# Performance work log

Hardware: AMD Instinct MI355X
Metric: run time of the kernel (lower is better)

## Reference

```python
import jax, jax.numpy as jnp
import numpy as np
import math

B, S, H, N = 1, 4096, 1024, 16
HN = H // N  # 64

def setup_inputs() -> dict:
    key = jax.random.key(0)
    k1, k2, k3 = jax.random.split(key, 3)
    hidden_states = jax.random.normal(k1, (B, S, H), dtype=jnp.float32)
    # lower-triangular causal mask, float {0,1}, broadcastable to [b,np,s,s]
    ltor_mask = jnp.tril(jnp.ones((1, 1, S, S), dtype=jnp.float32))
    w_qkv = jax.random.normal(k2, (3 * H, H), dtype=jnp.float32) * 0.02
    b_qkv = jnp.zeros((3 * H,), dtype=jnp.float32)
    w_dense = jax.random.normal(k3, (H, H), dtype=jnp.float32) * 0.02
    b_dense = jnp.zeros((H,), dtype=jnp.float32)
    return {"hidden_states": hidden_states, "ltor_mask": ltor_mask,
            "w_qkv": w_qkv, "b_qkv": b_qkv,
            "w_dense": w_dense, "b_dense": b_dense}

def reference(hidden_states, ltor_mask, w_qkv, b_qkv, w_dense, b_dense):
    b, s, h = hidden_states.shape
    # fused QKV projection: [b,s,3h]
    mixed = jnp.einsum('bsh,oh->bso', hidden_states, w_qkv) + b_qkv
    q, k, v = jnp.split(mixed, 3, axis=-1)
    # [b,s,h] -> [b,n,s,hn]
    def heads(t):
        return t.reshape(b, s, N, HN).transpose(0, 2, 1, 3)
    q, k, v = heads(q), heads(k), heads(v)
    # raw scores [b,n,s,s]
    scores = jnp.einsum('bnqd,bnkd->bnqk', q, k) / math.sqrt(HN)
    # multiplicative mask plus -10000 additive for masked positions
    scores = scores * ltor_mask - 10000.0 * (1.0 - ltor_mask)
    probs = jax.nn.softmax(scores, axis=-1)
    # attention dropout prob = 0.0 -> identity
    ctx = jnp.einsum('bnqk,bnkd->bnqd', probs, v)
    ctx = ctx.transpose(0, 2, 1, 3).reshape(b, s, h)
    out = jnp.einsum('bsh,oh->bso', ctx, w_dense) + b_dense
    # output dropout prob = 0.0 -> identity
    return out
```

## Files before the change

### kernel.cpp

```cpp
#include <hip/hip_runtime.h>
#include <hip/hip_bf16.h>

static constexpr int SEQ  = 4096;
static constexpr int HID  = 1024;
static constexpr int NHEAD = 16;
static constexpr int HDIM  = 64;
static constexpr int H3   = 3072;

typedef __attribute__((ext_vector_type(8))) __bf16 bf16x8;
typedef __attribute__((ext_vector_type(4))) float  f32x4;

__device__ __forceinline__ float bf2f(unsigned short u) {
    union { unsigned int u; float f; } v; v.u = ((unsigned int)u) << 16; return v.f;
}
__device__ __forceinline__ unsigned short f2bf(float f) {
    union { float f; unsigned int u; } v; v.f = f;
    unsigned int r = v.u + 0x7fffu + ((v.u >> 16) & 1u);
    return (unsigned short)(r >> 16);
}
__device__ __forceinline__ void gl_lds16(const unsigned short* g, unsigned short* l) {
    __builtin_amdgcn_global_load_lds(
        (const __attribute__((address_space(1))) void*)g,
        (__attribute__((address_space(3))) void*)l, 16, 0, 0);
}

struct Conv5 { const float* src[5]; unsigned short* dst[5]; };

__global__ __launch_bounds__(256) void convert5(Conv5 c) {
    constexpr int cnt[5]  = {4194304, 3145728, 3072, 1048576, 1024};
    constexpr int boff[5] = {0, 2048, 3584, 3586, 4098};
    const int b = blockIdx.x;
    int t = 0, rel = b;
#pragma unroll
    for (int k = 1; k < 5; ++k) if (b >= boff[k]) { t = k; rel = b - boff[k]; }
    const int base = rel * 2048 + threadIdx.x * 8;
    if (base >= cnt[t]) return;
    const float* s = c.src[t] + base;
    const float4 a = ((const float4*)s)[0];
    const float4 b2 = ((const float4*)s)[1];
    union { unsigned short v[8]; uint4 q; } u;
    u.v[0] = f2bf(a.x); u.v[1] = f2bf(a.y); u.v[2] = f2bf(a.z); u.v[3] = f2bf(a.w);
    u.v[4] = f2bf(b2.x); u.v[5] = f2bf(b2.y); u.v[6] = f2bf(b2.z); u.v[7] = f2bf(b2.w);
    *(uint4*)(c.dst[t] + base) = u.q;
}

template <int BM, int BN, int BK, typename OutT, bool VFUSE>
__global__ __launch_bounds__(256) void gemm_bt(
    const unsigned short* __restrict__ A, const unsigned short* __restrict__ B,
    const unsigned short* __restrict__ bias, OutT* __restrict__ C,
    unsigned short* __restrict__ vt,
    int M, int N, int K)
{
    constexpr int MI  = BM / 32;
    constexpr int NI  = BN / 32;
    constexpr int KC  = BK / 32;
    constexpr int CB  = BK / 8;
    constexpr int LSH = (BK == 32) ? 2 : 3;
    constexpr int RPC = 64 >> LSH;

    const int tid  = threadIdx.x;
    const int wave = tid >> 6, lane = tid & 63;
    const int quad = lane >> 4, c16 = lane & 15;
    const int m0 = blockIdx.y * BM, n0 = blockIdx.x * BN;
    const int wr = wave >> 1, wc = wave & 1;

    __shared__ __align__(16) unsigned short sA[BM * BK];
    __shared__ __align__(16) unsigned short sB[BN * BK];

    f32x4 acc[MI][NI];
#pragma unroll
    for (int i = 0; i < MI; ++i)
#pragma unroll
        for (int j = 0; j < NI; ++j) acc[i][j] = {0.f, 0.f, 0.f, 0.f};

    const int sr = lane >> LSH;
    const int sc = ((lane & (CB - 1)) ^ (sr & (CB - 1))) * 8;

    for (int k0 = 0; k0 < K; k0 += BK) {
#pragma unroll
        for (int cc = 0; cc < BM / RPC / 4; ++cc) {
            const int rbase = cc * (4 * RPC) + wave * RPC;
            gl_lds16(A + (size_t)(m0 + rbase + sr) * K + k0 + sc, &sA[rbase * BK]);
        }
#pragma unroll
        for (int cc = 0; cc < BN / RPC / 4; ++cc) {
            const int rbase = cc * (4 * RPC) + wave * RPC;
            gl_lds16(B + (size_t)(n0 + rbase + sr) * K + k0 + sc, &sB[rbase * BK]);
        }
        __syncthreads();

#pragma unroll
        for (int kc = 0; kc < KC; ++kc) {
            bf16x8 af[MI], bfr[NI];
#pragma unroll
            for (int i = 0; i < MI; ++i) {
                const int ra = wr * (BM / 2) + i * 16 + c16;
                af[i] = *(const bf16x8*)&sA[ra * BK + (((kc * 4 + quad) ^ ra) & (CB - 1)) * 8];
            }
#pragma unroll
            for (int j = 0; j < NI; ++j) {
                const int rb = wc * (BN / 2) + j * 16 + c16;
                bfr[j] = *(const bf16x8*)&sB[rb * BK + (((kc * 4 + quad) ^ rb) & (CB - 1)) * 8];
            }
#pragma unroll
            for (int i = 0; i < MI; ++i)
#pragma unroll
                for (int j = 0; j < NI; ++j)
                    acc[i][j] = __builtin_amdgcn_mfma_f32_16x16x32_bf16(af[i], bfr[j], acc[i][j], 0, 0, 0);
        }
        __syncthreads();
    }

    if constexpr (VFUSE) {
        if (n0 >= 2048) {
#pragma unroll
            for (int j = 0; j < NI; ++j) {
                const int col = n0 + wc * (BN / 2) + j * 16 + c16;
                const float bv = bf2f(bias[col]);
                const int d  = col - 2048;
                unsigned short* vrow = vt + (size_t)d * SEQ;
#pragma unroll
                for (int i = 0; i < MI; ++i) {
                    const int base32 = m0 + wr * (BM / 2) + (i >> 1) * 32;
                    const int phys = base32 + 8 * quad + 4 * (i & 1);
                    union { unsigned short u[4]; uint2 q2; } w;
#pragma unroll
                    for (int r = 0; r < 4; ++r) w.u[r] = f2bf(acc[i][j][r] + bv);
                    *(uint2*)&vrow[phys] = w.q2;
                }
            }
            return;
        }
    }

#pragma unroll
    for (int j = 0; j < NI; ++j) {
        const int col = n0 + wc * (BN / 2) + j * 16 + c16;
        const float bv = bf2f(bias[col]);
#pragma unroll
        for (int i = 0; i < MI; ++i) {
#pragma unroll
            for (int r = 0; r < 4; ++r) {
                const int row = m0 + wr * (BM / 2) + i * 16 + quad * 4 + r;
                const float v = acc[i][j][r] + bv;
                if constexpr (sizeof(OutT) == 2) C[(size_t)row * N + col] = (OutT)f2bf(v);
                else                             C[(size_t)row * N + col] = (OutT)v;
            }
        }
    }
}

__global__ __launch_bounds__(256) void attn_causal(
    const unsigned short* __restrict__ qkv, const unsigned short* __restrict__ vt,
    unsigned short* __restrict__ ctx)
{
    const int bx = blockIdx.x;
    const int n  = bx & 15;
    const int p  = bx >> 4;
    const int tid  = threadIdx.x;
    const int wave = tid >> 6, lane = tid & 63;
    const int quad = lane >> 4, c16 = lane & 15;
    const int qg  = wave & 1;
    const int kvh = wave >> 1;

    __shared__ __align__(16) unsigned short smem[16384];
    unsigned short* smem_k = smem;
    unsigned short* smem_v = smem + 8192;

    const float QS = 0.125f * 1.44269504f;
    const int srow8 = lane >> 3;
    const int scol8 = ((lane & 7) ^ (lane >> 3)) * 8;
    const int srow4 = lane >> 4;

#pragma unroll 1
    for (int t = 0; t < 2; ++t) {
        const int z = t ? p : 63 - p;
        const int qrow0 = z * 64 + qg * 32;

        bf16x8 qf[2][2];
#pragma unroll
        for (int wq = 0; wq < 2; ++wq)
#pragma unroll
            for (int kc = 0; kc < 2; ++kc) {
                bf16x8 q = *(const bf16x8*)(qkv + (size_t)(qrow0 + wq * 16 + c16) * H3 + n * HDIM + kc * 32 + quad * 8);
#pragma unroll
                for (int j = 0; j < 8; ++j) q[j] = (__bf16)((float)q[j] * QS);
                qf[wq][kc] = q;
            }

        f32x4 o[2][4];
#pragma unroll
        for (int wq = 0; wq < 2; ++wq)
#pragma unroll
            for (int dt = 0; dt < 4; ++dt) o[wq][dt] = {0.f, 0.f, 0.f, 0.f};
        float l_i[2] = {0.f, 0.f};

        const int nkb = (z + 2) >> 1;
        for (int kb = 0; kb < nkb; ++kb) {
            const int kv0 = kb * 128;
#pragma unroll
            for (int cc = 0; cc < 4; ++cc) {
                const int rb = wave * 32 + cc * 8;
                gl_lds16(qkv + (size_t)(kv0 + rb + srow8) * H3 + HID + n * HDIM + scol8,
                         &smem_k[rb * 64]);
            }
#pragma unroll
            for (int cc = 0; cc < 4; ++cc) {
                const int rb = wave * 16 + cc * 4;
                const int sv = (((lane & 15) ^ ((cc * 4 + srow4) & 15))) * 8;
                gl_lds16(vt + (size_t)(n * HDIM + rb + srow4) * SEQ + kv0 + sv,
                         &smem_v[rb * 128]);
            }
            __syncthreads();

            const int kv0w = kv0 + kvh * 64;
            if (kv0w <= qrow0 + 31) {
                f32x4 s[2][4];
#pragma unroll
                for (int wq = 0; wq < 2; ++wq)
#pragma unroll
                    for (int mt = 0; mt < 4; ++mt) s[wq][mt] = {0.f, 0.f, 0.f, 0.f};
#pragma unroll
                for (int mt = 0; mt < 4; ++mt) {
                    const int krow = kvh * 64 + mt * 16 + c16;
                    const bf16x8 kf0 = *(const bf16x8*)&smem_k[krow * 64 + ((quad)     ^ (krow & 7)) * 8];
                    const bf16x8 kf1 = *(const bf16x8*)&smem_k[krow * 64 + ((4 + quad) ^ (krow & 7)) * 8];
#pragma unroll
                    for (int wq = 0; wq < 2; ++wq) {
                        s[wq][mt] = __builtin_amdgcn_mfma_f32_16x16x32_bf16(kf0, qf[wq][0], s[wq][mt], 0, 0, 0);
                        s[wq][mt] = __builtin_amdgcn_mfma_f32_16x16x32_bf16(kf1, qf[wq][1], s[wq][mt], 0, 0, 0);
                    }
                }

#pragma unroll
                for (int wq = 0; wq < 2; ++wq) {
                    if (kv0w + 63 > qrow0 + wq * 16) {
                        const int q_g = qrow0 + wq * 16 + c16;
#pragma unroll
                        for (int mt = 0; mt < 4; ++mt)
#pragma unroll
                            for (int r = 0; r < 4; ++r) {
                                const int kv = kv0w + mt * 16 + quad * 4 + r;
                                if (kv > q_g) s[wq][mt][r] = -30000.0f;
                            }
                    }
                    float rs = 0.f;
#pragma unroll
                    for (int mt = 0; mt < 4; ++mt)
#pragma unroll
                        for (int r = 0; r < 4; ++r) {
                            const float pp = __builtin_amdgcn_exp2f(s[wq][mt][r]);
                            s[wq][mt][r] = pp;
                            rs += pp;
                        }
                    l_i[wq] += rs;
                }

                bf16x8 pf[2][2];
#pragma unroll
                for (int wq = 0; wq < 2; ++wq)
#pragma unroll
                    for (int kc = 0; kc < 2; ++kc) {
                        union { __bf16 b[8]; bf16x8 v; } pp;
#pragma unroll
                        for (int r = 0; r < 4; ++r) {
                            pp.b[r]     = (__bf16)s[wq][2 * kc][r];
                            pp.b[4 + r] = (__bf16)s[wq][2 * kc + 1][r];
                        }
                        pf[wq][kc] = pp.v;
                    }

#pragma unroll
                for (int kc = 0; kc < 2; ++kc) {
#pragma unroll
                    for (int dt = 0; dt < 4; ++dt) {
                        const int vrow = dt * 16 + c16;
                        const int pc8 = (kvh * 8 + kc * 4 + quad) ^ (vrow & 15);
                        const bf16x8 vf = *(const bf16x8*)&smem_v[vrow * 128 + pc8 * 8];
#pragma unroll
                        for (int wq = 0; wq < 2; ++wq)
                            o[wq][dt] = __builtin_amdgcn_mfma_f32_16x16x32_bf16(vf, pf[wq][kc], o[wq][dt], 0, 0, 0);
                    }
                }
            }
            __syncthreads();
        }

#pragma unroll
        for (int wq = 0; wq < 2; ++wq) {
            l_i[wq] += __shfl_xor(l_i[wq], 16);
            l_i[wq] += __shfl_xor(l_i[wq], 32);
        }

        float* cb = (float*)smem;
        float* lb = (float*)(smem + 8704);
        unsigned short* fb = smem + 8832;

        if (kvh == 0) {
#pragma unroll
            for (int wq = 0; wq < 2; ++wq) {
#pragma unroll
                for (int dt = 0; dt < 4; ++dt)
                    *(f32x4*)&cb[(qg * 32 + wq * 16 + c16) * 68 + dt * 16 + quad * 4] = o[wq][dt];
                if (quad == 0) lb[qg * 32 + wq * 16 + c16] = l_i[wq];
            }
        }
        __syncthreads();
        if (kvh == 1) {
#pragma unroll
            for (int wq = 0; wq < 2; ++wq) {
                const float inv = 1.0f / (l_i[wq] + lb[qg * 32 + wq * 16 + c16]);
#pragma unroll
                for (int dt = 0; dt < 4; ++dt) {
                    const f32x4 pv = *(const f32x4*)&cb[(qg * 32 + wq * 16 + c16) * 68 + dt * 16 + quad * 4];
                    union { unsigned short u[4]; uint2 q2; } w;
#pragma unroll
                    for (int r = 0; r < 4; ++r) w.u[r] = f2bf((o[wq][dt][r] + pv[r]) * inv);
                    *(uint2*)&fb[(qg * 32 + wq * 16 + c16) * 72 + dt * 16 + quad * 4] = w.q2;
                }
            }
        }
        __syncthreads();

        const int qr = tid >> 2;
        const int xc = (tid & 3) * 16;
        unsigned short* dst = ctx + (size_t)(z * 64 + qr) * HID + n * HDIM + xc;
        *(uint4*)dst       = *(const uint4*)&fb[qr * 72 + xc];
        *(uint4*)(dst + 8) = *(const uint4*)&fb[qr * 72 + xc + 8];

        __syncthreads();
    }
}

extern "C" void kernel_launch(void* const* d_in, const int* in_sizes, int n_in,
                              void* d_out, int out_size, void* d_ws, size_t ws_size,
                              hipStream_t stream)
{
    unsigned short* base = (unsigned short*)d_ws;

    unsigned short* hs_c = base;
    unsigned short* wq_c = hs_c + 4194304;
    unsigned short* bq_c = wq_c + 3145728;
    unsigned short* wd_c = bq_c + 3072;
    unsigned short* bd_c = wd_c + 1048576;
    unsigned short* qkv  = bd_c + 1024;
    unsigned short* vt   = qkv + (size_t)SEQ * H3;
    unsigned short* ctx  = hs_c;

    Conv5 c;
    c.src[0] = (const float*)d_in[0]; c.src[1] = (const float*)d_in[2];
    c.src[2] = (const float*)d_in[3]; c.src[3] = (const float*)d_in[4];
    c.src[4] = (const float*)d_in[5];
    c.dst[0] = hs_c; c.dst[1] = wq_c; c.dst[2] = bq_c; c.dst[3] = wd_c; c.dst[4] = bd_c;
    hipLaunchKernelGGL(convert5, dim3(4099), dim3(256), 0, stream, c);

    hipLaunchKernelGGL((gemm_bt<128, 128, 32, unsigned short, true>),
                       dim3(H3 / 128, SEQ / 128), dim3(256), 0, stream,
                       hs_c, wq_c, bq_c, qkv, vt, SEQ, H3, HID);
    hipLaunchKernelGGL(attn_causal, dim3(NHEAD * (SEQ / 128)), dim3(256), 0, stream,
                       qkv, vt, ctx);
    hipLaunchKernelGGL((gemm_bt<64, 128, 64, float, false>),
                       dim3(HID / 128, SEQ / 64), dim3(256), 0, stream,
                       ctx, wd_c, bd_c, (float*)d_out, (unsigned short*)nullptr, SEQ, HID, HID);
}
```

Before: 248.0 us.

## Drop LDS staging in attention, one query tile per block, deeper QKV GEMM K-tile

The attention kernel stops staging K and V tiles in shared memory behind block-wide barriers. Each wave now reads its K and V fragments straight from global memory, and each wave loops only over the key blocks its causal range needs, so waves no longer synchronise per key block. Each block now handles a single 64-row query tile instead of a balanced pair, which doubles the grid, and the tile order is remapped so heavy and light tiles interleave. The QKV GEMM K-tile is raised from 32 to 64. The risk is lower reuse of K and V, more global and L2 traffic, and uncoalesced strided loads.

```diff
diff --git a/kernel.cpp b/kernel.cpp
--- a/kernel.cpp
+++ b/kernel.cpp
@@ -156,180 +156,156 @@
 {
     const int bx = blockIdx.x;
     const int n  = bx & 15;
-    const int p  = bx >> 4;
+    const int z0 = bx >> 4;
+    const int z  = (z0 < 32) ? z0 : 95 - z0;
     const int tid  = threadIdx.x;
     const int wave = tid >> 6, lane = tid & 63;
     const int quad = lane >> 4, c16 = lane & 15;
     const int qg  = wave & 1;
     const int kvh = wave >> 1;
 
-    __shared__ __align__(16) unsigned short smem[16384];
-    unsigned short* smem_k = smem;
-    unsigned short* smem_v = smem + 8192;
+    __shared__ __align__(16) unsigned short smem[13440];
+
+    const int qrow0 = z * 64 + qg * 32;
 
     const float QS = 0.125f * 1.44269504f;
-    const int srow8 = lane >> 3;
-    const int scol8 = ((lane & 7) ^ (lane >> 3)) * 8;
-    const int srow4 = lane >> 4;
-
-#pragma unroll 1
-    for (int t = 0; t < 2; ++t) {
-        const int z = t ? p : 63 - p;
-        const int qrow0 = z * 64 + qg * 32;
-
-        bf16x8 qf[2][2];
+    bf16x8 qf[2][2];
+#pragma unroll
+    for (int wq = 0; wq < 2; ++wq)
+#pragma unroll
+        for (int kc = 0; kc < 2; ++kc) {
+            bf16x8 q = *(const bf16x8*)(qkv + (size_t)(qrow0 + wq * 16 + c16) * H3 + n * HDIM + kc * 32 + quad * 8);
+#pragma unroll
+            for (int j = 0; j < 8; ++j) q[j] = (__bf16)((float)q[j] * QS);
+            qf[wq][kc] = q;
+        }
+
+    f32x4 o[2][4];
+#pragma unroll
+    for (int wq = 0; wq < 2; ++wq)
+#pragma unroll
+        for (int dt = 0; dt < 4; ++dt) o[wq][dt] = {0.f, 0.f, 0.f, 0.f};
+    float l_i[2] = {0.f, 0.f};
+
+    const int Lq  = qrow0 + 31;
+    const int rel = Lq - kvh * 64;
+    const int nkb = (rel >= 0) ? (rel >> 7) + 1 : 0;
+
+    const unsigned short* kbase = qkv + HID + n * HDIM;
+    const unsigned short* vbase = vt + (size_t)(n * HDIM) * SEQ;
+
+    for (int kb = 0; kb < nkb; ++kb) {
+        const int kv0w = kb * 128 + kvh * 64;
+
+        f32x4 s[2][4];
 #pragma unroll
         for (int wq = 0; wq < 2; ++wq)
 #pragma unroll
+            for (int mt = 0; mt < 4; ++mt) s[wq][mt] = {0.f, 0.f, 0.f, 0.f};
+#pragma unroll
+        for (int mt = 0; mt < 4; ++mt) {
+            const unsigned short* kp = kbase + (size_t)(kv0w + mt * 16 + c16) * H3 + quad * 8;
+            const bf16x8 kf0 = *(const bf16x8*)kp;
+            const bf16x8 kf1 = *(const bf16x8*)(kp + 32);
+#pragma unroll
+            for (int wq = 0; wq < 2; ++wq) {
+                s[wq][mt] = __builtin_amdgcn_mfma_f32_16x16x32_bf16(kf0, qf[wq][0], s[wq][mt], 0, 0, 0);
+                s[wq][mt] = __builtin_amdgcn_mfma_f32_16x16x32_bf16(kf1, qf[wq][1], s[wq][mt], 0, 0, 0);
+            }
+        }
+
+#pragma unroll
+        for (int wq = 0; wq < 2; ++wq) {
+            if (kv0w + 63 > qrow0 + wq * 16) {
+                const int q_g = qrow0 + wq * 16 + c16;
+#pragma unroll
+                for (int mt = 0; mt < 4; ++mt)
+#pragma unroll
+                    for (int r = 0; r < 4; ++r) {
+                        const int kv = kv0w + mt * 16 + quad * 4 + r;
+                        if (kv > q_g) s[wq][mt][r] = -30000.0f;
+                    }
+            }
+            float rs = 0.f;
+#pragma unroll
+            for (int mt = 0; mt < 4; ++mt)
+#pragma unroll
+                for (int r = 0; r < 4; ++r) {
+                    const float pp = __builtin_amdgcn_exp2f(s[wq][mt][r]);
+                    s[wq][mt][r] = pp;
+                    rs += pp;
+                }
+            l_i[wq] += rs;
+        }
+
+        bf16x8 pf[2][2];
+#pragma unroll
+        for (int wq = 0; wq < 2; ++wq)
+#pragma unroll
             for (int kc = 0; kc < 2; ++kc) {
-                bf16x8 q = *(const bf16x8*)(qkv + (size_t)(qrow0 + wq * 16 + c16) * H3 + n * HDIM + kc * 32 + quad * 8);
-#pragma unroll
-                for (int j = 0; j < 8; ++j) q[j] = (__bf16)((float)q[j] * QS);
-                qf[wq][kc] = q;
-            }
-
-        f32x4 o[2][4];
-#pragma unroll
-        for (int wq = 0; wq < 2; ++wq)
-#pragma unroll
-            for (int dt = 0; dt < 4; ++dt) o[wq][dt] = {0.f, 0.f, 0.f, 0.f};
-        float l_i[2] = {0.f, 0.f};
-
-        const int nkb = (z + 2) >> 1;
-        for (int kb = 0; kb < nkb; ++kb) {
-            const int kv0 = kb * 128;
-#pragma unroll
-            for (int cc = 0; cc < 4; ++cc) {
-                const int rb = wave * 32 + cc * 8;
-                gl_lds16(qkv + (size_t)(kv0 + rb + srow8) * H3 + HID + n * HDIM + scol8,
-                         &smem_k[rb * 64]);
-            }
-#pragma unroll
-            for (int cc = 0; cc < 4; ++cc) {
-                const int rb = wave * 16 + cc * 4;
-                const int sv = (((lane & 15) ^ ((cc * 4 + srow4) & 15))) * 8;
-                gl_lds16(vt + (size_t)(n * HDIM + rb + srow4) * SEQ + kv0 + sv,
-                         &smem_v[rb * 128]);
-            }
-            __syncthreads();
-
-            const int kv0w = kv0 + kvh * 64;
-            if (kv0w <= qrow0 + 31) {
-                f32x4 s[2][4];
+                union { __bf16 b[8]; bf16x8 v; } pp;
+#pragma unroll
+                for (int r = 0; r < 4; ++r) {
+                    pp.b[r]     = (__bf16)s[wq][2 * kc][r];
+                    pp.b[4 + r] = (__bf16)s[wq][2 * kc + 1][r];
+                }
+                pf[wq][kc] = pp.v;
+            }
+
+#pragma unroll
+        for (int kc = 0; kc < 2; ++kc) {
+#pragma unroll
+            for (int dt = 0; dt < 4; ++dt) {
+                const int vrow = dt * 16 + c16;
+                const bf16x8 vf = *(const bf16x8*)(vbase + (size_t)vrow * SEQ + kv0w + kc * 32 + quad * 8);
 #pragma unroll
                 for (int wq = 0; wq < 2; ++wq)
-#pragma unroll
-                    for (int mt = 0; mt < 4; ++mt) s[wq][mt] = {0.f, 0.f, 0.f, 0.f};
-#pragma unroll
-                for (int mt = 0; mt < 4; ++mt) {
-                    const int krow = kvh * 64 + mt * 16 + c16;
-                    const bf16x8 kf0 = *(const bf16x8*)&smem_k[krow * 64 + ((quad)     ^ (krow & 7)) * 8];
-                    const bf16x8 kf1 = *(const bf16x8*)&smem_k[krow * 64 + ((4 + quad) ^ (krow & 7)) * 8];
-#pragma unroll
-                    for (int wq = 0; wq < 2; ++wq) {
-                        s[wq][mt] = __builtin_amdgcn_mfma_f32_16x16x32_bf16(kf0, qf[wq][0], s[wq][mt], 0, 0, 0);
-                        s[wq][mt] = __builtin_amdgcn_mfma_f32_16x16x32_bf16(kf1, qf[wq][1], s[wq][mt], 0, 0, 0);
-                    }
-                }
-
-#pragma unroll
-                for (int wq = 0; wq < 2; ++wq) {
-                    if (kv0w + 63 > qrow0 + wq * 16) {
-                        const int q_g = qrow0 + wq * 16 + c16;
-#pragma unroll
-                        for (int mt = 0; mt < 4; ++mt)
-#pragma unroll
-                            for (int r = 0; r < 4; ++r) {
-                                const int kv = kv0w + mt * 16 + quad * 4 + r;
-                                if (kv > q_g) s[wq][mt][r] = -30000.0f;
-                            }
-                    }
-                    float rs = 0.f;
-#pragma unroll
-                    for (int mt = 0; mt < 4; ++mt)
-#pragma unroll
-                        for (int r = 0; r < 4; ++r) {
-                            const float pp = __builtin_amdgcn_exp2f(s[wq][mt][r]);
-                            s[wq][mt][r] = pp;
-                            rs += pp;
-                        }
-                    l_i[wq] += rs;
-                }
-
-                bf16x8 pf[2][2];
-#pragma unroll
-                for (int wq = 0; wq < 2; ++wq)
-#pragma unroll
-                    for (int kc = 0; kc < 2; ++kc) {
-                        union { __bf16 b[8]; bf16x8 v; } pp;
-#pragma unroll
-                        for (int r = 0; r < 4; ++r) {
-                            pp.b[r]     = (__bf16)s[wq][2 * kc][r];
-                            pp.b[4 + r] = (__bf16)s[wq][2 * kc + 1][r];
-                        }
-                        pf[wq][kc] = pp.v;
-                    }
-
-#pragma unroll
-                for (int kc = 0; kc < 2; ++kc) {
-#pragma unroll
-                    for (int dt = 0; dt < 4; ++dt) {
-                        const int vrow = dt * 16 + c16;
-                        const int pc8 = (kvh * 8 + kc * 4 + quad) ^ (vrow & 15);
-                        const bf16x8 vf = *(const bf16x8*)&smem_v[vrow * 128 + pc8 * 8];
-#pragma unroll
-                        for (int wq = 0; wq < 2; ++wq)
-                            o[wq][dt] = __builtin_amdgcn_mfma_f32_16x16x32_bf16(vf, pf[wq][kc], o[wq][dt], 0, 0, 0);
-                    }
-                }
-            }
-            __syncthreads();
-        }
-
+                    o[wq][dt] = __builtin_amdgcn_mfma_f32_16x16x32_bf16(vf, pf[wq][kc], o[wq][dt], 0, 0, 0);
+            }
+        }
+    }
+
+#pragma unroll
+    for (int wq = 0; wq < 2; ++wq) {
+        l_i[wq] += __shfl_xor(l_i[wq], 16);
+        l_i[wq] += __shfl_xor(l_i[wq], 32);
+    }
+
+    float* cb = (float*)smem;
+    float* lb = (float*)(smem + 8704);
+    unsigned short* fb = smem + 8832;
+
+    if (kvh == 0) {
 #pragma unroll
         for (int wq = 0; wq < 2; ++wq) {
-            l_i[wq] += __shfl_xor(l_i[wq], 16);
-            l_i[wq] += __shfl_xor(l_i[wq], 32);
-        }
-
-        float* cb = (float*)smem;
-        float* lb = (float*)(smem + 8704);
-        unsigned short* fb = smem + 8832;
-
-        if (kvh == 0) {
-#pragma unroll
-            for (int wq = 0; wq < 2; ++wq) {
-#pragma unroll
-                for (int dt = 0; dt < 4; ++dt)
-                    *(f32x4*)&cb[(qg * 32 + wq * 16 + c16) * 68 + dt * 16 + quad * 4] = o[wq][dt];
-                if (quad == 0) lb[qg * 32 + wq * 16 + c16] = l_i[wq];
-            }
-        }
-        __syncthreads();
-        if (kvh == 1) {
-#pragma unroll
-            for (int wq = 0; wq < 2; ++wq) {
-                const float inv = 1.0f / (l_i[wq] + lb[qg * 32 + wq * 16 + c16]);
-#pragma unroll
-                for (int dt = 0; dt < 4; ++dt) {
-                    const f32x4 pv = *(const f32x4*)&cb[(qg * 32 + wq * 16 + c16) * 68 + dt * 16 + quad * 4];
-                    union { unsigned short u[4]; uint2 q2; } w;
-#pragma unroll
-                    for (int r = 0; r < 4; ++r) w.u[r] = f2bf((o[wq][dt][r] + pv[r]) * inv);
-                    *(uint2*)&fb[(qg * 32 + wq * 16 + c16) * 72 + dt * 16 + quad * 4] = w.q2;
-                }
-            }
-        }
-        __syncthreads();
-
-        const int qr = tid >> 2;
-        const int xc = (tid & 3) * 16;
-        unsigned short* dst = ctx + (size_t)(z * 64 + qr) * HID + n * HDIM + xc;
-        *(uint4*)dst       = *(const uint4*)&fb[qr * 72 + xc];
-        *(uint4*)(dst + 8) = *(const uint4*)&fb[qr * 72 + xc + 8];
-
-        __syncthreads();
-    }
+#pragma unroll
+            for (int dt = 0; dt < 4; ++dt)
+                *(f32x4*)&cb[(qg * 32 + wq * 16 + c16) * 68 + dt * 16 + quad * 4] = o[wq][dt];
+            if (quad == 0) lb[qg * 32 + wq * 16 + c16] = l_i[wq];
+        }
+    }
+    __syncthreads();
+    if (kvh == 1) {
+#pragma unroll
+        for (int wq = 0; wq < 2; ++wq) {
+            const float inv = 1.0f / (l_i[wq] + lb[qg * 32 + wq * 16 + c16]);
+#pragma unroll
+            for (int dt = 0; dt < 4; ++dt) {
+                const f32x4 pv = *(const f32x4*)&cb[(qg * 32 + wq * 16 + c16) * 68 + dt * 16 + quad * 4];
+                union { unsigned short u[4]; uint2 q2; } w;
+#pragma unroll
+                for (int r = 0; r < 4; ++r) w.u[r] = f2bf((o[wq][dt][r] + pv[r]) * inv);
+                *(uint2*)&fb[(qg * 32 + wq * 16 + c16) * 72 + dt * 16 + quad * 4] = w.q2;
+            }
+        }
+    }
+    __syncthreads();
+
+    const int qr = tid >> 2;
+    const int xc = (tid & 3) * 16;
+    unsigned short* dst = ctx + (size_t)(z * 64 + qr) * HID + n * HDIM + xc;
+    *(uint4*)dst       = *(const uint4*)&fb[qr * 72 + xc];
+    *(uint4*)(dst + 8) = *(const uint4*)&fb[qr * 72 + xc + 8];
 }
 
 extern "C" void kernel_launch(void* const* d_in, const int* in_sizes, int n_in,
@@ -354,10 +330,10 @@
     c.dst[0] = hs_c; c.dst[1] = wq_c; c.dst[2] = bq_c; c.dst[3] = wd_c; c.dst[4] = bd_c;
     hipLaunchKernelGGL(convert5, dim3(4099), dim3(256), 0, stream, c);
 
-    hipLaunchKernelGGL((gemm_bt<128, 128, 32, unsigned short, true>),
+    hipLaunchKernelGGL((gemm_bt<128, 128, 64, unsigned short, true>),
                        dim3(H3 / 128, SEQ / 128), dim3(256), 0, stream,
                        hs_c, wq_c, bq_c, qkv, vt, SEQ, H3, HID);
-    hipLaunchKernelGGL(attn_causal, dim3(NHEAD * (SEQ / 128)), dim3(256), 0, stream,
+    hipLaunchKernelGGL(attn_causal, dim3(NHEAD * (SEQ / 64)), dim3(256), 0, stream,
                        qkv, vt, ctx);
     hipLaunchKernelGGL((gemm_bt<64, 128, 64, float, false>),
                        dim3(HID / 128, SEQ / 64), dim3(256), 0, stream,
```

Measured after the change: 307.5 us. 1.24x slower.

## Double-buffer K/V tiles in attention, one query tile per block, raise QKV GEMM BK

Applied to the files above, without the earlier changes.

The attention kernel now launches one block per 64-row query tile, where each block previously handled a paired long and short tile. Blocks are ordered heaviest-first. K/V tiles are double-buffered in LDS so the next tile's global-to-LDS load is issued before computing on the current one, which removes one barrier per iteration. The MFMA sections get raised wave priority with s_setprio. The QKV GEMM K-tile grows from 32 to 64. The changes aim to overlap load latency with compute and improve load balance, at the cost of doubled LDS use (64KB per block), which may lower occupancy.

```diff
diff --git a/kernel.cpp b/kernel.cpp
--- a/kernel.cpp
+++ b/kernel.cpp
@@ -156,180 +156,188 @@
 {
     const int bx = blockIdx.x;
     const int n  = bx & 15;
-    const int p  = bx >> 4;
+    const int z  = 63 - (bx >> 4);
     const int tid  = threadIdx.x;
     const int wave = tid >> 6, lane = tid & 63;
     const int quad = lane >> 4, c16 = lane & 15;
     const int qg  = wave & 1;
     const int kvh = wave >> 1;
 
-    __shared__ __align__(16) unsigned short smem[16384];
-    unsigned short* smem_k = smem;
-    unsigned short* smem_v = smem + 8192;
+    __shared__ __align__(16) unsigned short smem[32768];
+
+    const int qrow0 = z * 64 + qg * 32;
 
     const float QS = 0.125f * 1.44269504f;
+    bf16x8 qf[2][2];
+#pragma unroll
+    for (int wq = 0; wq < 2; ++wq)
+#pragma unroll
+        for (int kc = 0; kc < 2; ++kc) {
+            bf16x8 q = *(const bf16x8*)(qkv + (size_t)(qrow0 + wq * 16 + c16) * H3 + n * HDIM + kc * 32 + quad * 8);
+#pragma unroll
+            for (int j = 0; j < 8; ++j) q[j] = (__bf16)((float)q[j] * QS);
+            qf[wq][kc] = q;
+        }
+
+    f32x4 o[2][4];
+#pragma unroll
+    for (int wq = 0; wq < 2; ++wq)
+#pragma unroll
+        for (int dt = 0; dt < 4; ++dt) o[wq][dt] = {0.f, 0.f, 0.f, 0.f};
+    float l_i[2] = {0.f, 0.f};
+
     const int srow8 = lane >> 3;
     const int scol8 = ((lane & 7) ^ (lane >> 3)) * 8;
     const int srow4 = lane >> 4;
 
-#pragma unroll 1
-    for (int t = 0; t < 2; ++t) {
-        const int z = t ? p : 63 - p;
-        const int qrow0 = z * 64 + qg * 32;
-
-        bf16x8 qf[2][2];
-#pragma unroll
-        for (int wq = 0; wq < 2; ++wq)
+    const int NK = (z + 2) >> 1;
+
+    auto stage = [&](int t, int kb) {
+        unsigned short* sk = smem + t * 16384;
+        unsigned short* sv = sk + 8192;
+        const int kv0 = kb * 128;
+#pragma unroll
+        for (int cc = 0; cc < 4; ++cc) {
+            const int rb = wave * 32 + cc * 8;
+            gl_lds16(qkv + (size_t)(kv0 + rb + srow8) * H3 + HID + n * HDIM + scol8,
+                     &sk[rb * 64]);
+        }
+#pragma unroll
+        for (int cc = 0; cc < 4; ++cc) {
+            const int rb = wave * 16 + cc * 4;
+            const int sv8 = (((lane & 15) ^ ((cc * 4 + srow4) & 15))) * 8;
+            gl_lds16(vt + (size_t)(n * HDIM + rb + srow4) * SEQ + kv0 + sv8,
+                     &sv[rb * 128]);
+        }
+    };
+
+    stage(0, 0);
+    __syncthreads();
+
+    for (int kb = 0; kb < NK; ++kb) {
+        if (kb + 1 < NK) stage((kb + 1) & 1, kb + 1);
+
+        unsigned short* smem_k = smem + (kb & 1) * 16384;
+        unsigned short* smem_v = smem_k + 8192;
+
+        const int kv0w = kb * 128 + kvh * 64;
+        if (kv0w <= qrow0 + 31) {
+            f32x4 s[2][4];
+#pragma unroll
+            for (int wq = 0; wq < 2; ++wq)
+#pragma unroll
+                for (int mt = 0; mt < 4; ++mt) s[wq][mt] = {0.f, 0.f, 0.f, 0.f};
+            __builtin_amdgcn_s_setprio(1);
+#pragma unroll
+            for (int mt = 0; mt < 4; ++mt) {
+                const int krow = kvh * 64 + mt * 16 + c16;
+                const bf16x8 kf0 = *(const bf16x8*)&smem_k[krow * 64 + ((quad)     ^ (krow & 7)) * 8];
+                const bf16x8 kf1 = *(const bf16x8*)&smem_k[krow * 64 + ((4 + quad) ^ (krow & 7)) * 8];
+#pragma unroll
+                for (int wq = 0; wq < 2; ++wq) {
+                    s[wq][mt] = __builtin_amdgcn_mfma_f32_16x16x32_bf16(kf0, qf[wq][0], s[wq][mt], 0, 0, 0);
+                    s[wq][mt] = __builtin_amdgcn_mfma_f32_16x16x32_bf16(kf1, qf[wq][1], s[wq][mt], 0, 0, 0);
+                }
+            }
+            __builtin_amdgcn_s_setprio(0);
+
+#pragma unroll
+            for (int wq = 0; wq < 2; ++wq) {
+                if (kv0w + 63 > qrow0 + wq * 16) {
+                    const int q_g = qrow0 + wq * 16 + c16;
+#pragma unroll
+                    for (int mt = 0; mt < 4; ++mt)
+#pragma unroll
+                        for (int r = 0; r < 4; ++r) {
+                            const int kv = kv0w + mt * 16 + quad * 4 + r;
+                            if (kv > q_g) s[wq][mt][r] = -30000.0f;
+                        }
+                }
+                float rs = 0.f;
+#pragma unroll
+                for (int mt = 0; mt < 4; ++mt)
+#pragma unroll
+                    for (int r = 0; r < 4; ++r) {
+                        const float pp = __builtin_amdgcn_exp2f(s[wq][mt][r]);
+                        s[wq][mt][r] = pp;
+                        rs += pp;
+                    }
+                l_i[wq] += rs;
+            }
+
+            bf16x8 pf[2][2];
+#pragma unroll
+            for (int wq = 0; wq < 2; ++wq)
+#pragma unroll
+                for (int kc = 0; kc < 2; ++kc) {
+                    union { __bf16 b[8]; bf16x8 v; } pp;
+#pragma unroll
+                    for (int r = 0; r < 4; ++r) {
+                        pp.b[r]     = (__bf16)s[wq][2 * kc][r];
+                        pp.b[4 + r] = (__bf16)s[wq][2 * kc + 1][r];
+                    }
+                    pf[wq][kc] = pp.v;
+                }
+
+            __builtin_amdgcn_s_setprio(1);
 #pragma unroll
             for (int kc = 0; kc < 2; ++kc) {
-                bf16x8 q = *(const bf16x8*)(qkv + (size_t)(qrow0 + wq * 16 + c16) * H3 + n * HDIM + kc * 32 + quad * 8);
-#pragma unroll
-                for (int j = 0; j < 8; ++j) q[j] = (__bf16)((float)q[j] * QS);
-                qf[wq][kc] = q;
-            }
-
-        f32x4 o[2][4];
-#pragma unroll
-        for (int wq = 0; wq < 2; ++wq)
-#pragma unroll
-            for (int dt = 0; dt < 4; ++dt) o[wq][dt] = {0.f, 0.f, 0.f, 0.f};
-        float l_i[2] = {0.f, 0.f};
-
-        const int nkb = (z + 2) >> 1;
-        for (int kb = 0; kb < nkb; ++kb) {
-            const int kv0 = kb * 128;
-#pragma unroll
-            for (int cc = 0; cc < 4; ++cc) {
-                const int rb = wave * 32 + cc * 8;
-                gl_lds16(qkv + (size_t)(kv0 + rb + srow8) * H3 + HID + n * HDIM + scol8,
-                         &smem_k[rb * 64]);
-            }
-#pragma unroll
-            for (int cc = 0; cc < 4; ++cc) {
-                const int rb = wave * 16 + cc * 4;
-                const int sv = (((lane & 15) ^ ((cc * 4 + srow4) & 15))) * 8;
-                gl_lds16(vt + (size_t)(n * HDIM + rb + srow4) * SEQ + kv0 + sv,
-                         &smem_v[rb * 128]);
-            }
-            __syncthreads();
-
-            const int kv0w = kv0 + kvh * 64;
-            if (kv0w <= qrow0 + 31) {
-                f32x4 s[2][4];
-#pragma unroll
-                for (int wq = 0; wq < 2; ++wq)
-#pragma unroll
-                    for (int mt = 0; mt < 4; ++mt) s[wq][mt] = {0.f, 0.f, 0.f, 0.f};
-#pragma unroll
-                for (int mt = 0; mt < 4; ++mt) {
-                    const int krow = kvh * 64 + mt * 16 + c16;
-                    const bf16x8 kf0 = *(const bf16x8*)&smem_k[krow * 64 + ((quad)     ^ (krow & 7)) * 8];
-                    const bf16x8 kf1 = *(const bf16x8*)&smem_k[krow * 64 + ((4 + quad) ^ (krow & 7)) * 8];
-#pragma unroll
-                    for (int wq = 0; wq < 2; ++wq) {
-                        s[wq][mt] = __builtin_amdgcn_mfma_f32_16x16x32_bf16(kf0, qf[wq][0], s[wq][mt], 0, 0, 0);
-                        s[wq][mt] = __builtin_amdgcn_mfma_f32_16x16x32_bf16(kf1, qf[wq][1], s[wq][mt], 0, 0, 0);
-                    }
-                }
-
-#pragma unroll
-                for (int wq = 0; wq < 2; ++wq) {
-                    if (kv0w + 63 > qrow0 + wq * 16) {
-                        const int q_g = qrow0 + wq * 16 + c16;
-#pragma unroll
-                        for (int mt = 0; mt < 4; ++mt)
-#pragma unroll
-                            for (int r = 0; r < 4; ++r) {
-                                const int kv = kv0w + mt * 16 + quad * 4 + r;
-                                if (kv > q_g) s[wq][mt][r] = -30000.0f;
-                            }
-                    }
-                    float rs = 0.f;
-#pragma unroll
-                    for (int mt = 0; mt < 4; ++mt)
-#pragma unroll
-                        for (int r = 0; r < 4; ++r) {
-                            const float pp = __builtin_amdgcn_exp2f(s[wq][mt][r]);
-                            s[wq][mt][r] = pp;
-                            rs += pp;
-                        }
-                    l_i[wq] += rs;
-                }
-
-                bf16x8 pf[2][2];
-#pragma unroll
-                for (int wq = 0; wq < 2; ++wq)
-#pragma unroll
-                    for (int kc = 0; kc < 2; ++kc) {
-                        union { __bf16 b[8]; bf16x8 v; } pp;
-#pragma unroll
-                        for (int r = 0; r < 4; ++r) {
-                            pp.b[r]     = (__bf16)s[wq][2 * kc][r];
-                            pp.b[4 + r] = (__bf16)s[wq][2 * kc + 1][r];
-                        }
-                        pf[wq][kc] = pp.v;
-                    }
-
-#pragma unroll
-                for (int kc = 0; kc < 2; ++kc) {
-#pragma unroll
-                    for (int dt = 0; dt < 4; ++dt) {
-                        const int vrow = dt * 16 + c16;
-                        const int pc8 = (kvh * 8 + kc * 4 + quad) ^ (vrow & 15);
-                        const bf16x8 vf = *(const bf16x8*)&smem_v[vrow * 128 + pc8 * 8];
-#pragma unroll
-                        for (int wq = 0; wq < 2; ++wq)
-                            o[wq][dt] = __builtin_amdgcn_mfma_f32_16x16x32_bf16(vf, pf[wq][kc], o[wq][dt], 0, 0, 0);
-                    }
-                }
-            }
-            __syncthreads();
-        }
-
+#pragma unroll
+                for (int dt = 0; dt < 4; ++dt) {
+                    const int vrow = dt * 16 + c16;
+                    const int pc8 = (kvh * 8 + kc * 4 + quad) ^ (vrow & 15);
+                    const bf16x8 vf = *(const bf16x8*)&smem_v[vrow * 128 + pc8 * 8];
+#pragma unroll
+                    for (int wq = 0; wq < 2; ++wq)
+                        o[wq][dt] = __builtin_amdgcn_mfma_f32_16x16x32_bf16(vf, pf[wq][kc], o[wq][dt], 0, 0, 0);
+                }
+            }
+            __builtin_amdgcn_s_setprio(0);
+        }
+        __syncthreads();
+    }
+
+#pragma unroll
+    for (int wq = 0; wq < 2; ++wq) {
+        l_i[wq] += __shfl_xor(l_i[wq], 16);
+        l_i[wq] += __shfl_xor(l_i[wq], 32);
+    }
+
+    float* cb = (float*)smem;
+    float* lb = (float*)(smem + 8704);
+    unsigned short* fb = smem + 8832;
+
+    if (kvh == 0) {
 #pragma unroll
         for (int wq = 0; wq < 2; ++wq) {
-            l_i[wq] += __shfl_xor(l_i[wq], 16);
-            l_i[wq] += __shfl_xor(l_i[wq], 32);
-        }
-
-        float* cb = (float*)smem;
-        float* lb = (float*)(smem + 8704);
-        unsigned short* fb = smem + 8832;
-
-        if (kvh == 0) {
-#pragma unroll
-            for (int wq = 0; wq < 2; ++wq) {
-#pragma unroll
-                for (int dt = 0; dt < 4; ++dt)
-                    *(f32x4*)&cb[(qg * 32 + wq * 16 + c16) * 68 + dt * 16 + quad * 4] = o[wq][dt];
-                if (quad == 0) lb[qg * 32 + wq * 16 + c16] = l_i[wq];
-            }
-        }
-        __syncthreads();
-        if (kvh == 1) {
-#pragma unroll
-            for (int wq = 0; wq < 2; ++wq) {
-                const float inv = 1.0f / (l_i[wq] + lb[qg * 32 + wq * 16 + c16]);
-#pragma unroll
-                for (int dt = 0; dt < 4; ++dt) {
-                    const f32x4 pv = *(const f32x4*)&cb[(qg * 32 + wq * 16 + c16) * 68 + dt * 16 + quad * 4];
-                    union { unsigned short u[4]; uint2 q2; } w;
-#pragma unroll
-                    for (int r = 0; r < 4; ++r) w.u[r] = f2bf((o[wq][dt][r] + pv[r]) * inv);
-                    *(uint2*)&fb[(qg * 32 + wq * 16 + c16) * 72 + dt * 16 + quad * 4] = w.q2;
-                }
-            }
-        }
-        __syncthreads();
-
-        const int qr = tid >> 2;
-        const int xc = (tid & 3) * 16;
-        unsigned short* dst = ctx + (size_t)(z * 64 + qr) * HID + n * HDIM + xc;
-        *(uint4*)dst       = *(const uint4*)&fb[qr * 72 + xc];
-        *(uint4*)(dst + 8) = *(const uint4*)&fb[qr * 72 + xc + 8];
-
-        __syncthreads();
-    }
+#pragma unroll
+            for (int dt = 0; dt < 4; ++dt)
+                *(f32x4*)&cb[(qg * 32 + wq * 16 + c16) * 68 + dt * 16 + quad * 4] = o[wq][dt];
+            if (quad == 0) lb[qg * 32 + wq * 16 + c16] = l_i[wq];
+        }
+    }
+    __syncthreads();
+    if (kvh == 1) {
+#pragma unroll
+        for (int wq = 0; wq < 2; ++wq) {
+            const float inv = 1.0f / (l_i[wq] + lb[qg * 32 + wq * 16 + c16]);
+#pragma unroll
+            for (int dt = 0; dt < 4; ++dt) {
+                const f32x4 pv = *(const f32x4*)&cb[(qg * 32 + wq * 16 + c16) * 68 + dt * 16 + quad * 4];
+                union { unsigned short u[4]; uint2 q2; } w;
+#pragma unroll
+                for (int r = 0; r < 4; ++r) w.u[r] = f2bf((o[wq][dt][r] + pv[r]) * inv);
+                *(uint2*)&fb[(qg * 32 + wq * 16 + c16) * 72 + dt * 16 + quad * 4] = w.q2;
+            }
+        }
+    }
+    __syncthreads();
+
+    const int qr = tid >> 2;
+    const int xc = (tid & 3) * 16;
+    unsigned short* dst = ctx + (size_t)(z * 64 + qr) * HID + n * HDIM + xc;
+    *(uint4*)dst       = *(const uint4*)&fb[qr * 72 + xc];
+    *(uint4*)(dst + 8) = *(const uint4*)&fb[qr * 72 + xc + 8];
 }
 
 extern "C" void kernel_launch(void* const* d_in, const int* in_sizes, int n_in,
@@ -354,10 +362,10 @@
     c.dst[0] = hs_c; c.dst[1] = wq_c; c.dst[2] = bq_c; c.dst[3] = wd_c; c.dst[4] = bd_c;
     hipLaunchKernelGGL(convert5, dim3(4099), dim3(256), 0, stream, c);
 
-    hipLaunchKernelGGL((gemm_bt<128, 128, 32, unsigned short, true>),
+    hipLaunchKernelGGL((gemm_bt<128, 128, 64, unsigned short, true>),
                        dim3(H3 / 128, SEQ / 128), dim3(256), 0, stream,
                        hs_c, wq_c, bq_c, qkv, vt, SEQ, H3, HID);
-    hipLaunchKernelGGL(attn_causal, dim3(NHEAD * (SEQ / 128)), dim3(256), 0, stream,
+    hipLaunchKernelGGL(attn_causal, dim3(NHEAD * (SEQ / 64)), dim3(256), 0, stream,
                        qkv, vt, ctx);
     hipLaunchKernelGGL((gemm_bt<64, 128, 64, float, false>),
                        dim3(HID / 128, SEQ / 64), dim3(256), 0, stream,
```

Result: faster. 240.4 us (-3.0%).

## Split heavy causal attention tiles across two blocks with partial reduction

Applied to the files above, without the earlier changes.

Causal attention no longer pairs a heavy and a light query tile inside one block; each block now handles a single query tile. The 33 heaviest tiles per head have their KV range split across two blocks, which write unnormalized partial outputs and row sums to a workspace buffer, and a new reduce kernel combines and normalizes them. The change also adds s_setprio around the MFMA sections, a minimum-occupancy launch bound, and a larger K tile for the QKV GEMM. The aim is better load balance and more parallelism across CUs, paid for with an extra launch and fp32 partial traffic, and it depends on the workspace being large enough.

```diff
diff --git a/kernel.cpp b/kernel.cpp
--- a/kernel.cpp
+++ b/kernel.cpp
@@ -150,13 +150,33 @@
     }
 }
 
-__global__ __launch_bounds__(256) void attn_causal(
+__global__ __launch_bounds__(256, 5) void attn_causal(
     const unsigned short* __restrict__ qkv, const unsigned short* __restrict__ vt,
-    unsigned short* __restrict__ ctx)
+    unsigned short* __restrict__ ctx, float* __restrict__ part, int split)
 {
     const int bx = blockIdx.x;
     const int n  = bx & 15;
-    const int p  = bx >> 4;
+    int z, kb0, kbN, heavy, pslot;
+    if (split) {
+        const int u = bx >> 4;
+        if (u < 66) {
+            z = 63 - (u >> 1);
+            const int nk = (z + 2) >> 1;
+            const int s0 = (nk + 1) >> 1;
+            const int c  = u & 1;
+            kb0 = c ? s0 : 0; kbN = c ? nk : s0;
+            heavy = 1; pslot = (n * 33 + (z - 31)) * 2 + c;
+        } else {
+            z = 96 - u;
+            kb0 = 0; kbN = (z + 2) >> 1;
+            heavy = 0; pslot = 0;
+        }
+    } else {
+        z = 63 - (bx >> 4);
+        kb0 = 0; kbN = (z + 2) >> 1;
+        heavy = 0; pslot = 0;
+    }
+
     const int tid  = threadIdx.x;
     const int wave = tid >> 6, lane = tid & 63;
     const int quad = lane >> 4, c16 = lane & 15;
@@ -167,146 +187,163 @@
     unsigned short* smem_k = smem;
     unsigned short* smem_v = smem + 8192;
 
+    const int qrow0 = z * 64 + qg * 32;
+
     const float QS = 0.125f * 1.44269504f;
+    bf16x8 qf[2][2];
+#pragma unroll
+    for (int wq = 0; wq < 2; ++wq)
+#pragma unroll
+        for (int kc = 0; kc < 2; ++kc) {
+            bf16x8 q = *(const bf16x8*)(qkv + (size_t)(qrow0 + wq * 16 + c16) * H3 + n * HDIM + kc * 32 + quad * 8);
+#pragma unroll
+            for (int j = 0; j < 8; ++j) q[j] = (__bf16)((float)q[j] * QS);
+            qf[wq][kc] = q;
+        }
+
+    f32x4 o[2][4];
+#pragma unroll
+    for (int wq = 0; wq < 2; ++wq)
+#pragma unroll
+        for (int dt = 0; dt < 4; ++dt) o[wq][dt] = {0.f, 0.f, 0.f, 0.f};
+    float l_i[2] = {0.f, 0.f};
+
     const int srow8 = lane >> 3;
     const int scol8 = ((lane & 7) ^ (lane >> 3)) * 8;
     const int srow4 = lane >> 4;
 
-#pragma unroll 1
-    for (int t = 0; t < 2; ++t) {
-        const int z = t ? p : 63 - p;
-        const int qrow0 = z * 64 + qg * 32;
-
-        bf16x8 qf[2][2];
-#pragma unroll
-        for (int wq = 0; wq < 2; ++wq)
+    for (int kb = kb0; kb < kbN; ++kb) {
+        const int kv0 = kb * 128;
+#pragma unroll
+        for (int cc = 0; cc < 4; ++cc) {
+            const int rb = wave * 32 + cc * 8;
+            gl_lds16(qkv + (size_t)(kv0 + rb + srow8) * H3 + HID + n * HDIM + scol8,
+                     &smem_k[rb * 64]);
+        }
+#pragma unroll
+        for (int cc = 0; cc < 4; ++cc) {
+            const int rb = wave * 16 + cc * 4;
+            const int sv = (((lane & 15) ^ ((cc * 4 + srow4) & 15))) * 8;
+            gl_lds16(vt + (size_t)(n * HDIM + rb + srow4) * SEQ + kv0 + sv,
+                     &smem_v[rb * 128]);
+        }
+        __syncthreads();
+
+        const int kv0w = kv0 + kvh * 64;
+        if (kv0w <= qrow0 + 31) {
+            f32x4 s[2][4];
+#pragma unroll
+            for (int wq = 0; wq < 2; ++wq)
+#pragma unroll
+                for (int mt = 0; mt < 4; ++mt) s[wq][mt] = {0.f, 0.f, 0.f, 0.f};
+            __builtin_amdgcn_s_setprio(1);
+#pragma unroll
+            for (int mt = 0; mt < 4; ++mt) {
+                const int krow = kvh * 64 + mt * 16 + c16;
+                const bf16x8 kf0 = *(const bf16x8*)&smem_k[krow * 64 + ((quad)     ^ (krow & 7)) * 8];
+                const bf16x8 kf1 = *(const bf16x8*)&smem_k[krow * 64 + ((4 + quad) ^ (krow & 7)) * 8];
+#pragma unroll
+                for (int wq = 0; wq < 2; ++wq) {
+                    s[wq][mt] = __builtin_amdgcn_mfma_f32_16x16x32_bf16(kf0, qf[wq][0], s[wq][mt], 0, 0, 0);
+                    s[wq][mt] = __builtin_amdgcn_mfma_f32_16x16x32_bf16(kf1, qf[wq][1], s[wq][mt], 0, 0, 0);
+                }
+            }
+            __builtin_amdgcn_s_setprio(0);
+
+#pragma unroll
+            for (int wq = 0; wq < 2; ++wq) {
+                if (kv0w + 63 > qrow0 + wq * 16) {
+                    const int q_g = qrow0 + wq * 16 + c16;
+#pragma unroll
+                    for (int mt = 0; mt < 4; ++mt)
+#pragma unroll
+                        for (int r = 0; r < 4; ++r) {
+                            const int kv = kv0w + mt * 16 + quad * 4 + r;
+                            if (kv > q_g) s[wq][mt][r] = -30000.0f;
+                        }
+                }
+                float rs = 0.f;
+#pragma unroll
+                for (int mt = 0; mt < 4; ++mt)
+#pragma unroll
+                    for (int r = 0; r < 4; ++r) {
+                        const float pp = __builtin_amdgcn_exp2f(s[wq][mt][r]);
+                        s[wq][mt][r] = pp;
+                        rs += pp;
+                    }
+                l_i[wq] += rs;
+            }
+
+            bf16x8 pf[2][2];
+#pragma unroll
+            for (int wq = 0; wq < 2; ++wq)
+#pragma unroll
+                for (int kc = 0; kc < 2; ++kc) {
+                    union { __bf16 b[8]; bf16x8 v; } pp;
+#pragma unroll
+                    for (int r = 0; r < 4; ++r) {
+                        pp.b[r]     = (__bf16)s[wq][2 * kc][r];
+                        pp.b[4 + r] = (__bf16)s[wq][2 * kc + 1][r];
+                    }
+                    pf[wq][kc] = pp.v;
+                }
+
+            __builtin_amdgcn_s_setprio(1);
 #pragma unroll
             for (int kc = 0; kc < 2; ++kc) {
-                bf16x8 q = *(const bf16x8*)(qkv + (size_t)(qrow0 + wq * 16 + c16) * H3 + n * HDIM + kc * 32 + quad * 8);
-#pragma unroll
-                for (int j = 0; j < 8; ++j) q[j] = (__bf16)((float)q[j] * QS);
-                qf[wq][kc] = q;
-            }
-
-        f32x4 o[2][4];
-#pragma unroll
-        for (int wq = 0; wq < 2; ++wq)
-#pragma unroll
-            for (int dt = 0; dt < 4; ++dt) o[wq][dt] = {0.f, 0.f, 0.f, 0.f};
-        float l_i[2] = {0.f, 0.f};
-
-        const int nkb = (z + 2) >> 1;
-        for (int kb = 0; kb < nkb; ++kb) {
-            const int kv0 = kb * 128;
-#pragma unroll
-            for (int cc = 0; cc < 4; ++cc) {
-                const int rb = wave * 32 + cc * 8;
-                gl_lds16(qkv + (size_t)(kv0 + rb + srow8) * H3 + HID + n * HDIM + scol8,
-                         &smem_k[rb * 64]);
-            }
-#pragma unroll
-            for (int cc = 0; cc < 4; ++cc) {
-                const int rb = wave * 16 + cc * 4;
-                const int sv = (((lane & 15) ^ ((cc * 4 + srow4) & 15))) * 8;
-                gl_lds16(vt + (size_t)(n * HDIM + rb + srow4) * SEQ + kv0 + sv,
-                         &smem_v[rb * 128]);
-            }
-            __syncthreads();
-
-            const int kv0w = kv0 + kvh * 64;
-            if (kv0w <= qrow0 + 31) {
-                f32x4 s[2][4];
-#pragma unroll
-                for (int wq = 0; wq < 2; ++wq)
-#pragma unroll
-                    for (int mt = 0; mt < 4; ++mt) s[wq][mt] = {0.f, 0.f, 0.f, 0.f};
-#pragma unroll
-                for (int mt = 0; mt < 4; ++mt) {
-                    const int krow = kvh * 64 + mt * 16 + c16;
-                    const bf16x8 kf0 = *(const bf16x8*)&smem_k[krow * 64 + ((quad)     ^ (krow & 7)) * 8];
-                    const bf16x8 kf1 = *(const bf16x8*)&smem_k[krow * 64 + ((4 + quad) ^ (krow & 7)) * 8];
-#pragma unroll
-                    for (int wq = 0; wq < 2; ++wq) {
-                        s[wq][mt] = __builtin_amdgcn_mfma_f32_16x16x32_bf16(kf0, qf[wq][0], s[wq][mt], 0, 0, 0);
-                        s[wq][mt] = __builtin_amdgcn_mfma_f32_16x16x32_bf16(kf1, qf[wq][1], s[wq][mt], 0, 0, 0);
-                    }
-                }
-
-#pragma unroll
-                for (int wq = 0; wq < 2; ++wq) {
-                    if (kv0w + 63 > qrow0 + wq * 16) {
-                        const int q_g = qrow0 + wq * 16 + c16;
-#pragma unroll
-                        for (int mt = 0; mt < 4; ++mt)
-#pragma unroll
-                            for (int r = 0; r < 4; ++r) {
-                                const int kv = kv0w + mt * 16 + quad * 4 + r;
-                                if (kv > q_g) s[wq][mt][r] = -30000.0f;
-                            }
-                    }
-                    float rs = 0.f;
-#pragma unroll
-                    for (int mt = 0; mt < 4; ++mt)
-#pragma unroll
-                        for (int r = 0; r < 4; ++r) {
-                            const float pp = __builtin_amdgcn_exp2f(s[wq][mt][r]);
-                            s[wq][mt][r] = pp;
-                            rs += pp;
-                        }
-                    l_i[wq] += rs;
-                }
-
-                bf16x8 pf[2][2];
-#pragma unroll
-                for (int wq = 0; wq < 2; ++wq)
-#pragma unroll
-                    for (int kc = 0; kc < 2; ++kc) {
-                        union { __bf16 b[8]; bf16x8 v; } pp;
-#pragma unroll
-                        for (int r = 0; r < 4; ++r) {
-                            pp.b[r]     = (__bf16)s[wq][2 * kc][r];
-                            pp.b[4 + r] = (__bf16)s[wq][2 * kc + 1][r];
-                        }
-                        pf[wq][kc] = pp.v;
-                    }
-
-#pragma unroll
-                for (int kc = 0; kc < 2; ++kc) {
-#pragma unroll
-                    for (int dt = 0; dt < 4; ++dt) {
-                        const int vrow = dt * 16 + c16;
-                        const int pc8 = (kvh * 8 + kc * 4 + quad) ^ (vrow & 15);
-                        const bf16x8 vf = *(const bf16x8*)&smem_v[vrow * 128 + pc8 * 8];
-#pragma unroll
-                        for (int wq = 0; wq < 2; ++wq)
-                            o[wq][dt] = __builtin_amdgcn_mfma_f32_16x16x32_bf16(vf, pf[wq][kc], o[wq][dt], 0, 0, 0);
-                    }
-                }
-            }
-            __syncthreads();
-        }
-
+#pragma unroll
+                for (int dt = 0; dt < 4; ++dt) {
+                    const int vrow = dt * 16 + c16;
+                    const int pc8 = (kvh * 8 + kc * 4 + quad) ^ (vrow & 15);
+                    const bf16x8 vf = *(const bf16x8*)&smem_v[vrow * 128 + pc8 * 8];
+#pragma unroll
+                    for (int wq = 0; wq < 2; ++wq)
+                        o[wq][dt] = __builtin_amdgcn_mfma_f32_16x16x32_bf16(vf, pf[wq][kc], o[wq][dt], 0, 0, 0);
+                }
+            }
+            __builtin_amdgcn_s_setprio(0);
+        }
+        __syncthreads();
+    }
+
+#pragma unroll
+    for (int wq = 0; wq < 2; ++wq) {
+        l_i[wq] += __shfl_xor(l_i[wq], 16);
+        l_i[wq] += __shfl_xor(l_i[wq], 32);
+    }
+
+    float* cb = (float*)smem;
+    float* lb = (float*)(smem + 8704);
+    unsigned short* fb = smem + 8832;
+
+    if (kvh == 0) {
 #pragma unroll
         for (int wq = 0; wq < 2; ++wq) {
-            l_i[wq] += __shfl_xor(l_i[wq], 16);
-            l_i[wq] += __shfl_xor(l_i[wq], 32);
-        }
-
-        float* cb = (float*)smem;
-        float* lb = (float*)(smem + 8704);
-        unsigned short* fb = smem + 8832;
-
-        if (kvh == 0) {
+#pragma unroll
+            for (int dt = 0; dt < 4; ++dt)
+                *(f32x4*)&cb[(qg * 32 + wq * 16 + c16) * 68 + dt * 16 + quad * 4] = o[wq][dt];
+            if (quad == 0) lb[qg * 32 + wq * 16 + c16] = l_i[wq];
+        }
+    }
+    __syncthreads();
+    if (kvh == 1) {
+        if (heavy) {
+            float* pb = part + (size_t)pslot * 4160;
 #pragma unroll
             for (int wq = 0; wq < 2; ++wq) {
-#pragma unroll
-                for (int dt = 0; dt < 4; ++dt)
-                    *(f32x4*)&cb[(qg * 32 + wq * 16 + c16) * 68 + dt * 16 + quad * 4] = o[wq][dt];
-                if (quad == 0) lb[qg * 32 + wq * 16 + c16] = l_i[wq];
-            }
-        }
-        __syncthreads();
-        if (kvh == 1) {
+                const int row = qg * 32 + wq * 16 + c16;
+                const float ls = l_i[wq] + lb[row];
+                if (quad == 0) pb[4096 + row] = ls;
+#pragma unroll
+                for (int dt = 0; dt < 4; ++dt) {
+                    const f32x4 pv = *(const f32x4*)&cb[row * 68 + dt * 16 + quad * 4];
+                    f32x4 os;
+#pragma unroll
+                    for (int r = 0; r < 4; ++r) os[r] = o[wq][dt][r] + pv[r];
+                    *(f32x4*)&pb[row * 64 + dt * 16 + quad * 4] = os;
+                }
+            }
+        } else {
 #pragma unroll
             for (int wq = 0; wq < 2; ++wq) {
                 const float inv = 1.0f / (l_i[wq] + lb[qg * 32 + wq * 16 + c16]);
@@ -320,16 +357,45 @@
                 }
             }
         }
-        __syncthreads();
-
+    }
+    __syncthreads();
+
+    if (!heavy) {
         const int qr = tid >> 2;
         const int xc = (tid & 3) * 16;
         unsigned short* dst = ctx + (size_t)(z * 64 + qr) * HID + n * HDIM + xc;
         *(uint4*)dst       = *(const uint4*)&fb[qr * 72 + xc];
         *(uint4*)(dst + 8) = *(const uint4*)&fb[qr * 72 + xc + 8];
-
-        __syncthreads();
-    }
+    }
+}
+
+__global__ __launch_bounds__(256) void reduce_heavy(
+    const float* __restrict__ part, unsigned short* __restrict__ ctx)
+{
+    const int bx = blockIdx.x;
+    const int n  = bx & 15;
+    const int zh = bx >> 4;
+    const int z  = 31 + zh;
+    const float* p0 = part + (size_t)((n * 33 + zh) * 2) * 4160;
+    const float* p1 = p0 + 4160;
+    const int r  = threadIdx.x >> 2;
+    const int sg = threadIdx.x & 3;
+
+    const float inv = 1.0f / (p0[4096 + r] + p1[4096 + r]);
+    union { unsigned short u[8]; uint4 q; } w0, w1;
+#pragma unroll
+    for (int j = 0; j < 8; ++j) {
+        const int idx = r * 64 + sg * 16 + j;
+        w0.u[j] = f2bf((p0[idx] + p1[idx]) * inv);
+    }
+#pragma unroll
+    for (int j = 0; j < 8; ++j) {
+        const int idx = r * 64 + sg * 16 + 8 + j;
+        w1.u[j] = f2bf((p0[idx] + p1[idx]) * inv);
+    }
+    unsigned short* dst = ctx + (size_t)(z * 64 + r) * HID + n * HDIM + sg * 16;
+    *(uint4*)dst       = w0.q;
+    *(uint4*)(dst + 8) = w1.q;
 }
 
 extern "C" void kernel_launch(void* const* d_in, const int* in_sizes, int n_in,
@@ -346,6 +412,10 @@
     unsigned short* qkv  = bd_c + 1024;
     unsigned short* vt   = qkv + (size_t)SEQ * H3;
     unsigned short* ctx  = hs_c;
+    float* part = (float*)(vt + 4194304);
+
+    const size_t need = (size_t)25169920 * 2 + (size_t)1056 * 4160 * 4;
+    const int split = (ws_size >= need) ? 1 : 0;
 
     Conv5 c;
     c.src[0] = (const float*)d_in[0]; c.src[1] = (const float*)d_in[2];
@@ -354,11 +424,17 @@
     c.dst[0] = hs_c; c.dst[1] = wq_c; c.dst[2] = bq_c; c.dst[3] = wd_c; c.dst[4] = bd_c;
     hipLaunchKernelGGL(convert5, dim3(4099), dim3(256), 0, stream, c);
 
-    hipLaunchKernelGGL((gemm_bt<128, 128, 32, unsigned short, true>),
+    hipLaunchKernelGGL((gemm_bt<128, 128, 64, unsigned short, true>),
                        dim3(H3 / 128, SEQ / 128), dim3(256), 0, stream,
                        hs_c, wq_c, bq_c, qkv, vt, SEQ, H3, HID);
-    hipLaunchKernelGGL(attn_causal, dim3(NHEAD * (SEQ / 128)), dim3(256), 0, stream,
-                       qkv, vt, ctx);
+
+    hipLaunchKernelGGL(attn_causal,
+                       dim3(split ? (97 * 16) : 1024), dim3(256), 0, stream,
+                       qkv, vt, ctx, part, split);
+    if (split)
+        hipLaunchKernelGGL(reduce_heavy, dim3(33 * 16), dim3(256), 0, stream,
+                           part, ctx);
+
     hipLaunchKernelGGL((gemm_bt<64, 128, 64, float, false>),
                        dim3(HID / 128, SEQ / 64), dim3(256), 0, stream,
                        ctx, wd_c, bd_c, (float*)d_out, (unsigned short*)nullptr, SEQ, HID, HID);
```

Measured after the change: 381.5 us. +53.8%, slower.
